# Kernel optimization log

Measured on AMD Instinct MI355X. Metric: run time of the kernel, lower is better.

Reference implementation:

```python
import jax, jax.numpy as jnp
import numpy as np

DIM, DH, H_HEADS, F, HH, WW = 512, 64, 8, 16, 32, 32
FF_IN = int(DIM * 4 * 2 / 3)  # 1365


def _ln(x, w, b):
    m = x.mean(-1, keepdims=True)
    v = ((x - m) ** 2).mean(-1, keepdims=True)
    return (x - m) * jax.lax.rsqrt(v + 1e-5) * w + b


def _attn(x, ln_w, ln_b, wq, wkv, nkv, nbias, wout, oln_w, oln_b, rel_bias):
    # x: (B, N, D); K/V are single-head (shared across heads) per the source to_kv
    B, N, D = x.shape
    H = nbias.shape[0]
    dh = nkv.shape[-1]
    xn = _ln(x, ln_w, ln_b)
    q = (xn @ wq).reshape(B, N, H, dh).transpose(0, 2, 1, 3) * (dh ** -0.5)
    k, v = jnp.split(xn @ wkv, 2, axis=-1)  # (B, N, dh) each
    nk = jnp.broadcast_to(nkv[0], (B, 1, dh))
    nv = jnp.broadcast_to(nkv[1], (B, 1, dh))
    k = jnp.concatenate([nk, k], axis=1)  # (B, N+1, dh)
    v = jnp.concatenate([nv, v], axis=1)
    sim = jnp.einsum('bhid,bjd->bhij', q, k)  # (B, H, N, N+1)
    bias = jnp.concatenate([jnp.broadcast_to(nbias[:, None, None], (H, N, 1)), rel_bias], axis=-1)
    attn = jax.nn.softmax(sim + bias[None], axis=-1)
    out = jnp.einsum('bhij,bjd->bhid', attn, v)
    out = out.transpose(0, 2, 1, 3).reshape(B, N, H * dh)
    return _ln(out @ wout, oln_w, oln_b)


def _cpb_mlp(coords, w0, b0, w1, b1, w2, b2):
    t = jax.nn.silu(coords @ w0 + b0)
    t = jax.nn.silu(t @ w1 + b1)
    return t @ w2 + b2  # (R, heads)


def _spatial_bias(h, w, w0, b0, w1, b1, w2, b2):
    rh = jnp.arange(-h + 1, h)
    rw = jnp.arange(-w + 1, w)
    gh, gw = jnp.meshgrid(rh, rw, indexing='ij')
    coords = jnp.stack([gh, gw], axis=-1).reshape(-1, 2).astype(jnp.float32)
    table = _cpb_mlp(coords, w0, b0, w1, b1, w2, b2)  # ((2h-1)(2w-1), H)
    ph, pw = jnp.meshgrid(jnp.arange(h), jnp.arange(w), indexing='ij')
    p = jnp.stack([ph, pw], axis=-1).reshape(-1, 2)  # (hw, 2)
    rel = p[:, None] - p[None]  # (hw, hw, 2)
    idx = (rel[..., 0] + h - 1) * (2 * w - 1) + (rel[..., 1] + w - 1)
    return table[idx].transpose(2, 0, 1)  # (H, hw, hw)


def _temporal_bias(f, w0, b0, w1, b1, w2, b2):
    coords = jnp.arange(-f + 1, f, dtype=jnp.float32)[:, None]
    table = _cpb_mlp(coords, w0, b0, w1, b1, w2, b2)  # (2f-1, H)
    idx = jnp.arange(f)[:, None] - jnp.arange(f)[None] + f - 1
    return table[idx].transpose(2, 0, 1)  # (H, f, f)


def _ff(x, win, g, wout):
    # 1x1x1 conv == channel matmul; GEGLU; shift_token; ChanLayerNorm; conv out
    y = jnp.einsum('bcfhw,cd->bdfhw', x, win)
    a, gate = jnp.split(y, 2, axis=1)
    y = a * jax.nn.gelu(gate, approximate=False)
    c = y.shape[1]
    c1 = (c + 1) // 2  # torch.chunk: first chunk gets ceil
    y1, y2 = y[:, :c1], y[:, c1:]
    y2 = jnp.pad(y2, ((0, 0), (0, 0), (1, 0), (0, 0), (0, 0)))[:, :, :-1]
    y = jnp.concatenate([y1, y2], axis=1)
    m = y.mean(1, keepdims=True)
    v = ((y - m) ** 2).mean(1, keepdims=True)
    y = (y - m) * jax.lax.rsqrt(jnp.maximum(v, 1e-5)) * g.reshape(1, -1, 1, 1, 1)
    return jnp.einsum('bcfhw,cd->bdfhw', y, wout)


def setup_inputs() -> dict:
    key = jax.random.key(0)
    ks = jax.random.split(key, 32)
    d2 = DIM // 2
    inner = DH * H_HEADS

    def nrm(k, shape, s=0.02):
        return jax.random.normal(k, shape, jnp.float32) * s

    inp = {'x': jax.random.normal(ks[0], (1, DIM, F, HH, WW), jnp.float32)}
    for pre, i in (('sa', 1), ('ta', 11)):
        inp[pre + '_ln_w'] = jnp.ones(DIM, jnp.float32)
        inp[pre + '_ln_b'] = jnp.zeros(DIM, jnp.float32)
        inp[pre + '_wq'] = nrm(ks[i], (DIM, inner))
        inp[pre + '_wkv'] = nrm(ks[i + 1], (DIM, 2 * DH))
        inp[pre + '_null_kv'] = nrm(ks[i + 2], (2, DH), 1.0)
        inp[pre + '_null_bias'] = nrm(ks[i + 3], (H_HEADS,), 1.0)
        inp[pre + '_wout'] = nrm(ks[i + 4], (inner, DIM))
        inp[pre + '_oln_w'] = jnp.ones(DIM, jnp.float32)
        inp[pre + '_oln_b'] = jnp.zeros(DIM, jnp.float32)
    inp['sp_w0'] = nrm(ks[20], (2, d2), 0.1); inp['sp_b0'] = jnp.zeros(d2, jnp.float32)
    inp['sp_w1'] = nrm(ks[21], (d2, d2), 0.05); inp['sp_b1'] = jnp.zeros(d2, jnp.float32)
    inp['sp_w2'] = nrm(ks[22], (d2, H_HEADS), 0.05); inp['sp_b2'] = jnp.zeros(H_HEADS, jnp.float32)
    inp['tp_w0'] = nrm(ks[23], (1, d2), 0.1); inp['tp_b0'] = jnp.zeros(d2, jnp.float32)
    inp['tp_w1'] = nrm(ks[24], (d2, d2), 0.05); inp['tp_b1'] = jnp.zeros(d2, jnp.float32)
    inp['tp_w2'] = nrm(ks[25], (d2, H_HEADS), 0.05); inp['tp_b2'] = jnp.zeros(H_HEADS, jnp.float32)
    inp['ff_win'] = nrm(ks[26], (DIM, 2 * FF_IN))
    inp['ff_g'] = jnp.ones(FF_IN, jnp.float32)
    inp['ff_wout'] = nrm(ks[27], (FF_IN, DIM))
    return inp


def _forward(x, sa_ln_w, sa_ln_b, sa_wq, sa_wkv, sa_null_kv, sa_null_bias, sa_wout, sa_oln_w, sa_oln_b,
             ta_ln_w, ta_ln_b, ta_wq, ta_wkv, ta_null_kv, ta_null_bias, ta_wout, ta_oln_w, ta_oln_b,
             sp_w0, sp_b0, sp_w1, sp_b1, sp_w2, sp_b2,
             tp_w0, tp_b0, tp_w1, tp_b1, tp_w2, tp_b2,
             ff_win, ff_g, ff_wout):
    b, c, f, h, w = x.shape
    # spatial attention over (h*w) tokens, batched over (b*f)
    xs = x.transpose(0, 2, 3, 4, 1).reshape(b * f, h * w, c)
    sb = _spatial_bias(h, w, sp_w0, sp_b0, sp_w1, sp_b1, sp_w2, sp_b2)
    xs = _attn(xs, sa_ln_w, sa_ln_b, sa_wq, sa_wkv, sa_null_kv, sa_null_bias, sa_wout, sa_oln_w, sa_oln_b, sb) + xs
    xv = xs.reshape(b, f, h, w, c).transpose(0, 4, 1, 2, 3)
    # temporal attention over f tokens, batched over (b*h*w)
    xt = xv.transpose(0, 3, 4, 2, 1).reshape(b * h * w, f, c)
    tb = _temporal_bias(f, tp_w0, tp_b0, tp_w1, tp_b1, tp_w2, tp_b2)
    xt = _attn(xt, ta_ln_w, ta_ln_b, ta_wq, ta_wkv, ta_null_kv, ta_null_bias, ta_wout, ta_oln_w, ta_oln_b, tb) + xt
    xv = xt.reshape(b, h, w, f, c).transpose(0, 4, 3, 1, 2)
    # feed-forward with token shift
    return _ff(xv, ff_win, ff_g, ff_wout) + xv


def reference(x, sa_ln_w, sa_ln_b, sa_wq, sa_wkv, sa_null_kv, sa_null_bias, sa_wout, sa_oln_w, sa_oln_b,
              ta_ln_w, ta_ln_b, ta_wq, ta_wkv, ta_null_kv, ta_null_bias, ta_wout, ta_oln_w, ta_oln_b,
              sp_w0, sp_b0, sp_w1, sp_b1, sp_w2, sp_b2,
              tp_w0, tp_b0, tp_w1, tp_b1, tp_w2, tp_b2,
              ff_win, ff_g, ff_wout):
    return _forward(x, sa_ln_w, sa_ln_b, sa_wq, sa_wkv, sa_null_kv, sa_null_bias, sa_wout, sa_oln_w, sa_oln_b,
                    ta_ln_w, ta_ln_b, ta_wq, ta_wkv, ta_null_kv, ta_null_bias, ta_wout, ta_oln_w, ta_oln_b,
                    sp_w0, sp_b0, sp_w1, sp_b1, sp_w2, sp_b2,
                    tp_w0, tp_b0, tp_w1, tp_b1, tp_w2, tp_b2,
                    ff_win, ff_g, ff_wout)
```

## Files before the change

kernel.cpp:

```cpp
#include <hip/hip_runtime.h>
#include <math.h>

#define TOK 16384
#define DIMC 512
#define FFI 1365
#define CH1 683
#define YSLD 1376
#define KVPAD 1056
#define BSTRIDE 1152
#define MASKB (-30000.f)
#define LOG2E 1.4426950408889634f

typedef unsigned int u32;
typedef unsigned short ushort_t;
typedef __attribute__((ext_vector_type(8))) short bf16x8;
typedef __attribute__((ext_vector_type(4))) float f32x4;

__device__ inline ushort_t f2b(float x) {
    u32 u = __float_as_uint(x);
    u32 r = (u + 0x7fffu + ((u >> 16) & 1u)) >> 16;
    return (ushort_t)r;
}
__device__ inline float b2f(ushort_t u) { return __uint_as_float(((u32)u) << 16); }

__device__ inline float exp2_fast(float x) {
    float r;
    asm("v_exp_f32 %0, %1" : "=v"(r) : "v"(x));
    return r;
}

__device__ inline u32 cvt_pk_bf16(float lo, float hi) {
    u32 r;
    asm("v_cvt_pk_bf16_f32 %0, %1, %2" : "=v"(r) : "v"(lo), "v"(hi));
    return r;
}

__device__ inline void gload_lds16(const void* g, void* l) {
    __builtin_amdgcn_global_load_lds(
        (const __attribute__((address_space(1))) u32*)g,
        (__attribute__((address_space(3))) u32*)l, 16, 0, 0);
}

__device__ inline float gelu_exact(float x) {
    return 0.5f * x * (1.f + erff(x * 0.70710678118654752f));
}

__device__ inline void waitcnt_vm4() {
    asm volatile("s_waitcnt vmcnt(4)" ::: "memory");
    __builtin_amdgcn_sched_barrier(0);
}
__device__ inline void waitcnt_vm0() {
    asm volatile("s_waitcnt vmcnt(0)" ::: "memory");
    __builtin_amdgcn_sched_barrier(0);
}

__global__ __launch_bounds__(256) void cpb_kernel(
    const float* __restrict__ w0, const float* __restrict__ b0,
    const float* __restrict__ w1, const float* __restrict__ b1,
    const float* __restrict__ w2, const float* __restrict__ b2,
    float* __restrict__ table, int mode)
{
    __shared__ float t0[256];
    __shared__ float t1[256];
    int r = blockIdx.x;
    int t = threadIdx.x;
    float c0, c1;
    if (mode == 0) { c0 = (float)(r / 63 - 31); c1 = (float)(r % 63 - 31); }
    else           { c0 = (float)(r - 15);      c1 = 0.f; }
    float a = c0 * w0[t] + b0[t];
    if (mode == 0) a += c1 * w0[256 + t];
    t0[t] = a / (1.f + __expf(-a));
    __syncthreads();
    float s = b1[t];
    for (int k = 0; k < 256; ++k) s += t0[k] * w1[k * 256 + t];
    t1[t] = s / (1.f + __expf(-s));
    __syncthreads();
    if (t < 8) {
        float o = b2[t];
        for (int k = 0; k < 256; ++k) o += t1[k] * w2[k * 8 + t];
        table[r * 8 + t] = o;
    }
}

__global__ __launch_bounds__(256) void bias_sp_kernel(
    const float* __restrict__ tab, const float* __restrict__ nullbias,
    ushort_t* __restrict__ out)
{
    int pi = blockIdx.x, h = blockIdx.y;
    int phi = pi >> 5, pwi = pi & 31;
    ushort_t* row = out + ((size_t)h * 1024 + pi) * BSTRIDE;
    for (int c = threadIdx.x; c < BSTRIDE; c += 256) {
        float v;
        if (c == 0) v = nullbias[h];
        else if (c <= 1024) {
            int pj = c - 1;
            int phj = pj >> 5, pwj = pj & 31;
            int idx = (phi - phj + 31) * 63 + (pwi - pwj + 31);
            v = tab[idx * 8 + h];
        } else v = MASKB;
        row[c] = f2b(v * LOG2E);
    }
}

__global__ __launch_bounds__(256) void kvinit_kernel(
    const float* __restrict__ nullkv, ushort_t* __restrict__ KP, ushort_t* __restrict__ VT)
{
    int f = blockIdx.x, t = threadIdx.x;
    for (int e = t; e < 32 * 64; e += 256) {
        int rr = e >> 6, d = e & 63;
        int row = (rr == 0) ? 0 : (1024 + rr);
        KP[((size_t)f * KVPAD + row) * 64 + d] = (rr == 0) ? f2b(nullkv[d]) : (ushort_t)0;
    }
    for (int e = t; e < 64 * 32; e += 256) {
        int d = e >> 5, cc = e & 31;
        int col = (cc == 0) ? 0 : (1024 + cc);
        VT[((size_t)f * 64 + d) * KVPAD + col] = (cc == 0) ? f2b(nullkv[64 + d]) : (ushort_t)0;
    }
}

__global__ __launch_bounds__(256) void wcvt_kernel(
    const float* __restrict__ W, int ldw, int c0,
    ushort_t* __restrict__ Bt, int Kp, int K, int Ncols,
    const float* __restrict__ gv, int Nwrite)
{
    __shared__ float tile[32][33];
    int nb = blockIdx.x * 32, kb = blockIdx.y * 32;
    int tx = threadIdx.x & 31, ty = threadIdx.x >> 5;
    #pragma unroll
    for (int it = 0; it < 4; ++it) {
        int k = kb + ty + it * 8, n = nb + tx;
        float v = (k < K && n < Ncols) ? W[(size_t)k * ldw + c0 + n] : 0.f;
        if (gv && k < K) v *= gv[k];
        tile[ty + it * 8][tx] = v;
    }
    __syncthreads();
    #pragma unroll
    for (int it = 0; it < 4; ++it) {
        int n = nb + ty + it * 8, k = kb + tx;
        if (n < Nwrite && k < Kp) Bt[(size_t)n * Kp + k] = f2b(tile[tx][ty + it * 8]);
    }
}

__global__ __launch_bounds__(256) void transpose_in_kernel(
    const float* __restrict__ x, float* __restrict__ dst)
{
    __shared__ float tile[32][33];
    int t0b = blockIdx.x * 32, c0b = blockIdx.y * 32;
    int tx = threadIdx.x & 31, ty = threadIdx.x >> 5;
    #pragma unroll
    for (int it = 0; it < 4; ++it) {
        int c = ty + it * 8;
        tile[c][tx] = x[(size_t)(c0b + c) * TOK + t0b + tx];
    }
    __syncthreads();
    #pragma unroll
    for (int it = 0; it < 4; ++it) {
        int tr = ty + it * 8;
        dst[(size_t)(t0b + tr) * DIMC + c0b + tx] = tile[tx][tr];
    }
}

__global__ __launch_bounds__(256) void ln_bf16_kernel(
    const float* __restrict__ in, ushort_t* __restrict__ out,
    const float* __restrict__ w, const float* __restrict__ b)
{
    __shared__ float r1[4], r2[4];
    size_t base = (size_t)blockIdx.x * DIMC;
    int t = threadIdx.x;
    float x0 = in[base + t], x1 = in[base + 256 + t];
    float s = x0 + x1, s2 = x0 * x0 + x1 * x1;
    #pragma unroll
    for (int o = 32; o > 0; o >>= 1) { s += __shfl_down(s, o, 64); s2 += __shfl_down(s2, o, 64); }
    if ((t & 63) == 0) { r1[t >> 6] = s; r2[t >> 6] = s2; }
    __syncthreads();
    float mean = (r1[0] + r1[1] + r1[2] + r1[3]) * (1.f / 512.f);
    float ex2  = (r2[0] + r2[1] + r2[2] + r2[3]) * (1.f / 512.f);
    float rstd = rsqrtf(ex2 - mean * mean + 1e-5f);
    out[base + t]       = f2b((x0 - mean) * rstd * w[t] + b[t]);
    out[base + 256 + t] = f2b((x1 - mean) * rstd * w[256 + t] + b[256 + t]);
}

__global__ __launch_bounds__(256) void ln_add_kernel(
    const float* __restrict__ proj, float* __restrict__ io,
    const float* __restrict__ w, const float* __restrict__ b)
{
    __shared__ float r1[4], r2[4];
    size_t base = (size_t)blockIdx.x * DIMC;
    int t = threadIdx.x;
    float x0 = proj[base + t], x1 = proj[base + 256 + t];
    float s = x0 + x1, s2 = x0 * x0 + x1 * x1;
    #pragma unroll
    for (int o = 32; o > 0; o >>= 1) { s += __shfl_down(s, o, 64); s2 += __shfl_down(s2, o, 64); }
    if ((t & 63) == 0) { r1[t >> 6] = s; r2[t >> 6] = s2; }
    __syncthreads();
    float mean = (r1[0] + r1[1] + r1[2] + r1[3]) * (1.f / 512.f);
    float ex2  = (r2[0] + r2[1] + r2[2] + r2[3]) * (1.f / 512.f);
    float rstd = rsqrtf(ex2 - mean * mean + 1e-5f);
    io[base + t]       += (x0 - mean) * rstd * w[t] + b[t];
    io[base + 256 + t] += (x1 - mean) * rstd * w[256 + t] + b[256 + t];
}

__global__ __launch_bounds__(128) void permute0_kernel(
    const float* __restrict__ src, float* __restrict__ dst)
{
    int rd = blockIdx.x;
    int rs = (rd & 15) * 1024 + (rd >> 4);
    ((float4*)(dst + (size_t)rd * DIMC))[threadIdx.x] =
        ((const float4*)(src + (size_t)rs * DIMC))[threadIdx.x];
}

__global__ __launch_bounds__(128) void permute1_dual_kernel(
    const float* __restrict__ src, float* __restrict__ dst, ushort_t* __restrict__ dstb)
{
    int rd = blockIdx.x;
    int rs = (rd & 1023) * 16 + (rd >> 10);
    float4 v = ((const float4*)(src + (size_t)rs * DIMC))[threadIdx.x];
    ((float4*)(dst + (size_t)rd * DIMC))[threadIdx.x] = v;
    u32 lo = (u32)f2b(v.x) | ((u32)f2b(v.y) << 16);
    u32 hi = (u32)f2b(v.z) | ((u32)f2b(v.w) << 16);
    ((uint2*)(dstb + (size_t)rd * DIMC))[threadIdx.x] = make_uint2(lo, hi);
}

template<int EPI>
__global__ __launch_bounds__(256) void gemm_mfma(
    const ushort_t* __restrict__ A, int lda,
    const ushort_t* __restrict__ Bt, int Kp,
    float* __restrict__ C, ushort_t* __restrict__ Cb, int ldc,
    int M, int N, int K, float scale, int nx,
    const float* __restrict__ stats, const float* __restrict__ g,
    const float* __restrict__ resid, float* __restrict__ outT,
    ushort_t* __restrict__ KPo, ushort_t* __restrict__ VTo)
{
    __shared__ __align__(16) ushort_t As[2][4 * 128 * 8];
    __shared__ __align__(16) ushort_t Bs[2][4 * 128 * 8];
    int lin = blockIdx.x;
    int xcd = lin & 7, idx = lin >> 3;
    int m0 = (xcd * 16 + (idx & 15)) * 128;
    int n0 = (idx >> 4) * 128;
    int tid = threadIdx.x, lane = tid & 63, wid = tid >> 6;
    int wy = wid >> 1, wx = wid & 1, quad = lane >> 4, l16 = lane & 15;
    bool bfull = (n0 + 128 <= N);
    f32x4 acc[4][4];
    #pragma unroll
    for (int i = 0; i < 4; ++i)
        #pragma unroll
        for (int j = 0; j < 4; ++j) { acc[i][j][0]=0.f; acc[i][j][1]=0.f; acc[i][j][2]=0.f; acc[i][j][3]=0.f; }

    auto stageA = [&](int buf, int k0) {
        #pragma unroll
        for (int r = 0; r < 2; ++r) {
            int c = wid * 128 + r * 64 + lane;
            const ushort_t* src = A + (size_t)(m0 + (c & 127)) * lda + k0 + (c >> 7) * 8;
            gload_lds16(src, &As[buf][(wid * 128 + r * 64) * 8]);
        }
    };
    auto stageB = [&](int buf, int k0) {
        #pragma unroll
        for (int r = 0; r < 2; ++r) {
            int c = wid * 128 + r * 64 + lane;
            const ushort_t* src = Bt + (size_t)(n0 + (c & 127)) * Kp + k0 + (c >> 7) * 8;
            gload_lds16(src, &Bs[buf][(wid * 128 + r * 64) * 8]);
        }
    };

    if (bfull) {
        int NT = K >> 5;
        stageA(0, 0); stageB(0, 0);
        if (NT > 1) { stageA(1, 32); stageB(1, 32); }
        for (int t = 0; t < NT; ++t) {
            if (t + 1 < NT) waitcnt_vm4(); else waitcnt_vm0();
            __builtin_amdgcn_s_barrier();
            int cur = t & 1;
            bf16x8 af[4], bfr[4];
            #pragma unroll
            for (int i = 0; i < 4; ++i) af[i] = *(bf16x8*)&As[cur][(quad * 128 + wy * 64 + i * 16 + l16) * 8];
            #pragma unroll
            for (int j = 0; j < 4; ++j) bfr[j] = *(bf16x8*)&Bs[cur][(quad * 128 + wx * 64 + j * 16 + l16) * 8];
            #pragma unroll
            for (int i = 0; i < 4; ++i)
                #pragma unroll
                for (int j = 0; j < 4; ++j)
                    acc[i][j] = __builtin_amdgcn_mfma_f32_16x16x32_bf16(af[i], bfr[j], acc[i][j], 0, 0, 0);
            if (t + 2 < NT) {
                __builtin_amdgcn_s_barrier();
                stageA(cur, (t + 2) * 32); stageB(cur, (t + 2) * 32);
            }
        }
    } else {
        for (int k0 = 0; k0 < K; k0 += 32) {
            if (k0) __syncthreads();
            stageA(0, k0);
            #pragma unroll
            for (int r = 0; r < 2; ++r) {
                int c = tid + r * 256;
                int kg = c >> 7, nloc = c & 127;
                bf16x8 v;
                if (n0 + nloc < N) v = *(const bf16x8*)(Bt + (size_t)(n0 + nloc) * Kp + k0 + kg * 8);
                else { for (int e = 0; e < 8; ++e) v[e] = 0; }
                *(bf16x8*)&Bs[0][c * 8] = v;
            }
            __syncthreads();
            bf16x8 af[4], bfr[4];
            #pragma unroll
            for (int i = 0; i < 4; ++i) af[i] = *(bf16x8*)&As[0][(quad * 128 + wy * 64 + i * 16 + l16) * 8];
            #pragma unroll
            for (int j = 0; j < 4; ++j) bfr[j] = *(bf16x8*)&Bs[0][(quad * 128 + wx * 64 + j * 16 + l16) * 8];
            #pragma unroll
            for (int i = 0; i < 4; ++i)
                #pragma unroll
                for (int j = 0; j < 4; ++j)
                    acc[i][j] = __builtin_amdgcn_mfma_f32_16x16x32_bf16(af[i], bfr[j], acc[i][j], 0, 0, 0);
        }
    }
    #pragma unroll
    for (int i = 0; i < 4; ++i) {
        #pragma unroll
        for (int j = 0; j < 4; ++j) {
            #pragma unroll
            for (int r = 0; r < 4; ++r) {
                int m = m0 + wy * 64 + i * 16 + quad * 4 + r;
                int n = n0 + wx * 64 + j * 16 + l16;
                if (n >= N) continue;
                float v = acc[i][j][r] * scale;
                if (EPI == 0) {
                    C[(size_t)m * ldc + n] = v;
                } else if (EPI == 3) {
                    Cb[(size_t)m * ldc + n] = f2b(v);
                } else if (EPI == 4) {
                    int frame = m >> 10, tt = m & 1023;
                    if (n < 64) KPo[((size_t)frame * KVPAD + 1 + tt) * 64 + n] = f2b(v);
                    else        VTo[((size_t)frame * 64 + (n - 64)) * KVPAD + 1 + tt] = f2b(v);
                } else if (EPI == 5) {
                    float s0 = stats[2 * m], s1 = stats[2 * m + 1];
                    outT[(size_t)n * TOK + m] = v * s1 - s0 * g[n] + resid[(size_t)m * DIMC + n];
                }
            }
        }
    }
}

__global__ __launch_bounds__(256) void ff_gemm_fused(
    const ushort_t* __restrict__ A,
    const ushort_t* __restrict__ BI,
    ushort_t* __restrict__ YS)
{
    __shared__ __align__(16) ushort_t As[2][4 * 128 * 8];
    __shared__ __align__(16) ushort_t Bs[2][4 * 2 * 64 * 8];
    int lin = blockIdx.x;
    int xcd = lin & 7, idx = lin >> 3;
    int m0 = (xcd * 16 + (idx & 15)) * 128;
    int n0 = (idx >> 4) * 64;
    int tid = threadIdx.x, lane = tid & 63, wid = tid >> 6;
    int wy = wid >> 1, wx = wid & 1, quad = lane >> 4, l16 = lane & 15;
    f32x4 aA[4][2], aG[4][2];
    #pragma unroll
    for (int i = 0; i < 4; ++i)
        #pragma unroll
        for (int j = 0; j < 2; ++j) {
            aA[i][j][0]=0.f; aA[i][j][1]=0.f; aA[i][j][2]=0.f; aA[i][j][3]=0.f;
            aG[i][j][0]=0.f; aG[i][j][1]=0.f; aG[i][j][2]=0.f; aG[i][j][3]=0.f;
        }

    auto stage = [&](int buf, int k0) {
        #pragma unroll
        for (int r = 0; r < 2; ++r) {
            int c = wid * 128 + r * 64 + lane;
            gload_lds16(A + (size_t)(m0 + (c & 127)) * 512 + k0 + (c >> 7) * 8,
                        &As[buf][(wid * 128 + r * 64) * 8]);
        }
        #pragma unroll
        for (int r = 0; r < 2; ++r) {
            gload_lds16(BI + (size_t)((n0 + lane) * 2 + r) * 512 + k0 + wid * 8,
                        &Bs[buf][(wid * 128 + r * 64) * 8]);
        }
    };

    stage(0, 0);
    stage(1, 32);
    for (int t = 0; t < 16; ++t) {
        if (t + 1 < 16) waitcnt_vm4(); else waitcnt_vm0();
        __builtin_amdgcn_s_barrier();
        int cur = t & 1;
        bf16x8 af[4], ba[2], bg[2];
        #pragma unroll
        for (int i = 0; i < 4; ++i) af[i] = *(bf16x8*)&As[cur][(quad * 128 + wy * 64 + i * 16 + l16) * 8];
        #pragma unroll
        for (int j = 0; j < 2; ++j) {
            int nn = wx * 32 + j * 16 + l16;
            ba[j] = *(bf16x8*)&Bs[cur][(quad * 128 + nn) * 8];
            bg[j] = *(bf16x8*)&Bs[cur][(quad * 128 + 64 + nn) * 8];
        }
        #pragma unroll
        for (int i = 0; i < 4; ++i)
            #pragma unroll
            for (int j = 0; j < 2; ++j) {
                aA[i][j] = __builtin_amdgcn_mfma_f32_16x16x32_bf16(af[i], ba[j], aA[i][j], 0, 0, 0);
                aG[i][j] = __builtin_amdgcn_mfma_f32_16x16x32_bf16(af[i], bg[j], aG[i][j], 0, 0, 0);
            }
        if (t + 2 < 16) {
            __builtin_amdgcn_s_barrier();
            stage(cur, (t + 2) * 32);
        }
    }
    #pragma unroll
    for (int i = 0; i < 4; ++i) {
        #pragma unroll
        for (int j = 0; j < 2; ++j) {
            #pragma unroll
            for (int r = 0; r < 4; ++r) {
                int m = m0 + wy * 64 + i * 16 + quad * 4 + r;
                int n = n0 + wx * 32 + j * 16 + l16;
                if (n >= FFI) {
                    if (n < YSLD) YS[(size_t)m * YSLD + n] = 0;
                    continue;
                }
                float v = aA[i][j][r] * gelu_exact(aG[i][j][r]);
                int dr = (n < CH1) ? m : m + 1024;
                if (dr < TOK) YS[(size_t)dr * YSLD + n] = f2b(v);
                if (n >= CH1 && m < 1024) YS[(size_t)m * YSLD + n] = 0;
            }
        }
    }
}

__global__ __launch_bounds__(256) void attn_sp_mfma(
    const ushort_t* __restrict__ Q,
    const ushort_t* __restrict__ KP,
    const ushort_t* __restrict__ VT,
    const ushort_t* __restrict__ BIASX,
    ushort_t* __restrict__ O)
{
    __shared__ __align__(16) ushort_t Ks[128 * 64];
    __shared__ __align__(16) ushort_t Vs[64 * 128];
    int lin = blockIdx.x;
    int xcd = lin & 7, idx = lin >> 3;
    int qt = xcd * 8 + (idx & 7);
    int frame = idx >> 3;
    int q0 = qt * 16;
    int tid = threadIdx.x, lane = tid & 63, wid = tid >> 6;
    int quad = lane >> 4, l16 = lane & 15;

    bf16x8 aQ[2][2];
    const ushort_t* brow[2];
    #pragma unroll
    for (int i = 0; i < 2; ++i) {
        int h = wid * 2 + i;
        const ushort_t* qp = Q + (size_t)(frame * 1024 + q0 + l16) * 512 + h * 64 + quad * 8;
        aQ[i][0] = *(const bf16x8*)qp;
        aQ[i][1] = *(const bf16x8*)(qp + 32);
        brow[i] = BIASX + ((size_t)h * 1024 + q0 + l16) * BSTRIDE;
    }
    f32x4 Oc[2][4];
    f32x4 Oc4[2];
    #pragma unroll
    for (int i = 0; i < 2; ++i) {
        #pragma unroll
        for (int nt = 0; nt < 4; ++nt) { Oc[i][nt][0]=0.f; Oc[i][nt][1]=0.f; Oc[i][nt][2]=0.f; Oc[i][nt][3]=0.f; }
        Oc4[i][0]=0.f; Oc4[i][1]=0.f; Oc4[i][2]=0.f; Oc4[i][3]=0.f;
    }
    bf16x8 vones;
    #pragma unroll
    for (int e = 0; e < 8; ++e) vones[e] = (short)0x3F80;

    int idxA = (((quad & 1) * 32) + l16) * 4;
    int idxB = idxA + 64;
    bool hiq = (quad >= 2);

    for (int jt = 0; jt < 9; ++jt) {
        __syncthreads();
        #pragma unroll
        for (int r = 0; r < 4; ++r) {
            int L = wid * 256 + r * 64 + lane;
            int c = L >> 3, gp = L & 7, gg = gp ^ (c & 7);
            int jj = jt * 128 + c; if (jj > KVPAD - 1) jj = KVPAD - 1;
            gload_lds16(KP + ((size_t)frame * KVPAD + jj) * 64 + gg * 8, &Ks[(wid * 256 + r * 64) * 8]);
        }
        #pragma unroll
        for (int r = 0; r < 4; ++r) {
            int L = wid * 256 + r * 64 + lane;
            int d = L >> 4, cgp = L & 15;
            int cg = (cgp & 8) | ((cgp & 7) ^ (d & 7));
            int col = jt * 128 + cg * 8; if (col > KVPAD - 8) col = KVPAD - 8;
            gload_lds16(VT + ((size_t)frame * 64 + d) * KVPAD + col, &Vs[(wid * 256 + r * 64) * 8]);
        }
        __syncthreads();

        #pragma unroll
        for (int i = 0; i < 2; ++i) {
            f32x4 S[8];
            #pragma unroll
            for (int j = 0; j < 8; ++j) { S[j][0]=0.f; S[j][1]=0.f; S[j][2]=0.f; S[j][3]=0.f; }
            __builtin_amdgcn_s_setprio(1);
            #pragma unroll
            for (int j = 0; j < 8; ++j) {
                int c = j * 16 + l16;
                #pragma unroll
                for (int ks = 0; ks < 2; ++ks) {
                    bf16x8 kb = *(bf16x8*)&Ks[(c * 8 + ((ks * 4 + quad) ^ (c & 7))) * 8];
                    S[j] = __builtin_amdgcn_mfma_f32_16x16x32_bf16(kb, aQ[i][ks], S[j], 0, 0, 0);
                }
            }
            __builtin_amdgcn_s_setprio(0);
            #pragma unroll
            for (int j = 0; j < 8; ++j) {
                int kbase = jt * 128 + j * 16 + quad * 4;
                uint2 bv = *(const uint2*)(brow[i] + kbase);
                S[j][0] = exp2_fast(S[j][0] + __uint_as_float(bv.x << 16));
                S[j][1] = exp2_fast(S[j][1] + __uint_as_float(bv.x & 0xffff0000u));
                S[j][2] = exp2_fast(S[j][2] + __uint_as_float(bv.y << 16));
                S[j][3] = exp2_fast(S[j][3] + __uint_as_float(bv.y & 0xffff0000u));
            }
            __builtin_amdgcn_s_setprio(1);
            #pragma unroll
            for (int ks = 0; ks < 4; ++ks) {
                int jl = 2 * ks, jh = 2 * ks + 1;
                u32 pxl = cvt_pk_bf16(S[jl][0], S[jl][1]);
                u32 pyl = cvt_pk_bf16(S[jl][2], S[jl][3]);
                u32 pxh = cvt_pk_bf16(S[jh][0], S[jh][1]);
                u32 pyh = cvt_pk_bf16(S[jh][2], S[jh][3]);
                u32 a0 = (u32)__builtin_amdgcn_ds_bpermute(idxA, (int)pxl);
                u32 a1 = (u32)__builtin_amdgcn_ds_bpermute(idxA, (int)pxh);
                u32 b0 = (u32)__builtin_amdgcn_ds_bpermute(idxA, (int)pyl);
                u32 b1 = (u32)__builtin_amdgcn_ds_bpermute(idxA, (int)pyh);
                u32 c0 = (u32)__builtin_amdgcn_ds_bpermute(idxB, (int)pxl);
                u32 c1 = (u32)__builtin_amdgcn_ds_bpermute(idxB, (int)pxh);
                u32 d0 = (u32)__builtin_amdgcn_ds_bpermute(idxB, (int)pyl);
                u32 d1 = (u32)__builtin_amdgcn_ds_bpermute(idxB, (int)pyh);
                union { u32 w[4]; bf16x8 v; } pa;
                pa.w[0] = hiq ? a1 : a0;
                pa.w[1] = hiq ? b1 : b0;
                pa.w[2] = hiq ? c1 : c0;
                pa.w[3] = hiq ? d1 : d0;
                #pragma unroll
                for (int nt = 0; nt < 4; ++nt) {
                    int d = nt * 16 + l16;
                    int cg = ks * 4 + quad;
                    int phys = (cg & 8) | ((cg & 7) ^ (d & 7));
                    bf16x8 vb = *(bf16x8*)&Vs[(d * 16 + phys) * 8];
                    Oc[i][nt] = __builtin_amdgcn_mfma_f32_16x16x32_bf16(pa.v, vb, Oc[i][nt], 0, 0, 0);
                }
                Oc4[i] = __builtin_amdgcn_mfma_f32_16x16x32_bf16(pa.v, vones, Oc4[i], 0, 0, 0);
            }
            __builtin_amdgcn_s_setprio(0);
        }
    }
    #pragma unroll
    for (int i = 0; i < 2; ++i) {
        int h = wid * 2 + i;
        #pragma unroll
        for (int r = 0; r < 4; ++r) {
            float linv = 1.f / Oc4[i][r];
            int ql = quad * 4 + r;
            #pragma unroll
            for (int nt = 0; nt < 4; ++nt) {
                int d = nt * 16 + l16;
                O[(size_t)(frame * 1024 + q0 + ql) * 512 + h * 64 + d] = f2b(Oc[i][nt][r] * linv);
            }
        }
    }
}

__global__ __launch_bounds__(256) void attn_tp_kernel(
    const ushort_t* __restrict__ q, const ushort_t* __restrict__ kv,
    const float* __restrict__ nullkv, const float* __restrict__ nullbias,
    const float* __restrict__ table, ushort_t* __restrict__ out)
{
    __shared__ float qs[16][512];
    __shared__ float ks[17][64];
    __shared__ float vs[17][64];
    __shared__ float sc[8][16][17];
    int b = blockIdx.x;
    int t = threadIdx.x;
    for (int e = t; e < 16 * 512; e += 256) {
        int f = e >> 9, c = e & 511;
        qs[f][c] = b2f(q[(size_t)(b * 16 + f) * 512 + c]);
    }
    for (int e = t; e < 17 * 64; e += 256) {
        int j = e >> 6, d = e & 63;
        ks[j][d] = (j == 0) ? nullkv[d]      : b2f(kv[(size_t)(b * 16 + j - 1) * 128 + d]);
        vs[j][d] = (j == 0) ? nullkv[64 + d] : b2f(kv[(size_t)(b * 16 + j - 1) * 128 + 64 + d]);
    }
    __syncthreads();
    for (int e = t; e < 8 * 16 * 17; e += 256) {
        int h = e / 272, rem = e - h * 272;
        int i = rem / 17, j = rem - i * 17;
        float acc = 0.f;
        for (int d = 0; d < 64; ++d) acc += qs[i][h * 64 + d] * ks[j][d];
        float bias = ((j == 0) ? nullbias[h] : table[(i - (j - 1) + 15) * 8 + h]) * LOG2E;
        sc[h][i][j] = acc + bias;
    }
    __syncthreads();
    if (t < 128) {
        int h = t >> 4, i = t & 15;
        float mx = -1e30f;
        for (int j = 0; j < 17; ++j) mx = fmaxf(mx, sc[h][i][j]);
        float s = 0.f;
        for (int j = 0; j < 17; ++j) { float p = exp2_fast(sc[h][i][j] - mx); sc[h][i][j] = p; s += p; }
        float inv = 1.f / s;
        for (int j = 0; j < 17; ++j) sc[h][i][j] *= inv;
    }
    __syncthreads();
    for (int e = t; e < 16 * 512; e += 256) {
        int i = e >> 9, c = e & 511;
        int h = c >> 6, d = c & 63;
        float acc = 0.f;
        #pragma unroll
        for (int j = 0; j < 17; ++j) acc += sc[h][i][j] * vs[j][d];
        out[(size_t)(b * 16 + i) * 512 + c] = f2b(acc);
    }
}

__global__ __launch_bounds__(256) void rowstats_bf16_kernel(
    const ushort_t* __restrict__ YS, float* __restrict__ stats)
{
    __shared__ float r1[4], r2[4];
    int r = blockIdx.x, t = threadIdx.x;
    const ushort_t* row = YS + (size_t)r * YSLD;
    float s = 0.f, s2 = 0.f;
    for (int c = t; c < FFI; c += 256) {
        float v = b2f(row[c]);
        s += v; s2 += v * v;
    }
    #pragma unroll
    for (int o = 32; o > 0; o >>= 1) { s += __shfl_down(s, o, 64); s2 += __shfl_down(s2, o, 64); }
    if ((t & 63) == 0) { r1[t >> 6] = s; r2[t >> 6] = s2; }
    __syncthreads();
    float S  = r1[0] + r1[1] + r1[2] + r1[3];
    float S2 = r2[0] + r2[1] + r2[2] + r2[3];
    float mean = S * (1.f / 1365.f);
    float var  = S2 * (1.f / 1365.f) - mean * mean;
    float rstd = rsqrtf(fmaxf(var, 1e-5f));
    if (t == 0) { stats[2 * r] = mean * rstd; stats[2 * r + 1] = rstd; }
}

__global__ __launch_bounds__(64) void colsum_kernel(
    const ushort_t* __restrict__ Wt, float* __restrict__ colsum)
{
    int n = blockIdx.x, t = threadIdx.x;
    const ushort_t* row = Wt + (size_t)n * YSLD;
    float s = 0.f;
    for (int k = t; k < YSLD; k += 64) s += b2f(row[k]);
    #pragma unroll
    for (int o = 32; o > 0; o >>= 1) s += __shfl_down(s, o, 64);
    if (t == 0) colsum[n] = s;
}

extern "C" void kernel_launch(void* const* d_in, const int* in_sizes, int n_in,
                              void* d_out, int out_size, void* d_ws, size_t ws_size,
                              hipStream_t stream)
{
    const float* x          = (const float*)d_in[0];
    const float* sa_ln_w    = (const float*)d_in[1];
    const float* sa_ln_b    = (const float*)d_in[2];
    const float* sa_wq      = (const float*)d_in[3];
    const float* sa_wkv     = (const float*)d_in[4];
    const float* sa_null_kv = (const float*)d_in[5];
    const float* sa_null_b  = (const float*)d_in[6];
    const float* sa_wout    = (const float*)d_in[7];
    const float* sa_oln_w   = (const float*)d_in[8];
    const float* sa_oln_b   = (const float*)d_in[9];
    const float* ta_ln_w    = (const float*)d_in[10];
    const float* ta_ln_b    = (const float*)d_in[11];
    const float* ta_wq      = (const float*)d_in[12];
    const float* ta_wkv     = (const float*)d_in[13];
    const float* ta_null_kv = (const float*)d_in[14];
    const float* ta_null_b  = (const float*)d_in[15];
    const float* ta_wout    = (const float*)d_in[16];
    const float* ta_oln_w   = (const float*)d_in[17];
    const float* ta_oln_b   = (const float*)d_in[18];
    const float* sp_w0      = (const float*)d_in[19];
    const float* sp_b0      = (const float*)d_in[20];
    const float* sp_w1      = (const float*)d_in[21];
    const float* sp_b1      = (const float*)d_in[22];
    const float* sp_w2      = (const float*)d_in[23];
    const float* sp_b2      = (const float*)d_in[24];
    const float* tp_w0      = (const float*)d_in[25];
    const float* tp_b0      = (const float*)d_in[26];
    const float* tp_w1      = (const float*)d_in[27];
    const float* tp_b1      = (const float*)d_in[28];
    const float* tp_w2      = (const float*)d_in[29];
    const float* tp_b2      = (const float*)d_in[30];
    const float* ff_win     = (const float*)d_in[31];
    const float* ff_g       = (const float*)d_in[32];
    const float* ff_wout    = (const float*)d_in[33];

    char* ws = (char*)d_ws;
    float*    RES   = (float*)(ws + 0);
    ushort_t* XN16  = (ushort_t*)(ws + 33554432);
    ushort_t* Q16   = (ushort_t*)(ws + 50331648);
    float*    RT    = (float*)(ws + 50331648);
    ushort_t* YS    = (ushort_t*)(ws + 50331648);
    ushort_t* WSA   = (ushort_t*)(ws + 67108864);
    ushort_t* KP    = (ushort_t*)(ws + 83886080);
    ushort_t* VTb   = (ushort_t*)(ws + 86048768);
    ushort_t* KV16  = (ushort_t*)(ws + 83886080);
    ushort_t* WTA   = (ushort_t*)(ws + 90439680);
    ushort_t* AO16  = (ushort_t*)(ws + 92274688);
    ushort_t* BI    = (ushort_t*)(ws + 96468992);
    ushort_t* WFFB  = (ushort_t*)(ws + 99352576);
    ushort_t* BIAS16= (ushort_t*)(ws + 109051904);
    float*    PRJ   = (float*)(ws + 109051904);
    ushort_t* Q16t  = (ushort_t*)(ws + 109051904);
    float*    STATS = (float*)(ws + 142606336);
    float*    SPT   = (float*)(ws + 142737408);
    float*    COLSUM= (float*)(ws + 142737408);
    float*    TPT   = (float*)(ws + 142864448);

    ushort_t* WQ_T  = WSA;
    ushort_t* WKV_T = WSA + 262144;
    ushort_t* WO_T  = WSA + 327680;
    ushort_t* tWQ_T  = WTA;
    ushort_t* tWKV_T = WTA + 262144;
    ushort_t* tWO_T  = WTA + 327680;

    dim3 blk(256);
    const float QSCL = 0.125f * LOG2E;

    cpb_kernel<<<dim3(3969), blk, 0, stream>>>(sp_w0, sp_b0, sp_w1, sp_b1, sp_w2, sp_b2, SPT, 0);
    cpb_kernel<<<dim3(31),   blk, 0, stream>>>(tp_w0, tp_b0, tp_w1, tp_b1, tp_w2, tp_b2, TPT, 1);
    bias_sp_kernel<<<dim3(1024, 8), blk, 0, stream>>>(SPT, sa_null_b, BIAS16);
    kvinit_kernel<<<dim3(16), blk, 0, stream>>>(sa_null_kv, KP, VTb);

    wcvt_kernel<<<dim3(16, 16), blk, 0, stream>>>(sa_wq, 512, 0, WQ_T, 512, 512, 512, nullptr, 512);
    wcvt_kernel<<<dim3(4, 16),  blk, 0, stream>>>(sa_wkv, 128, 0, WKV_T, 512, 512, 128, nullptr, 128);
    wcvt_kernel<<<dim3(16, 16), blk, 0, stream>>>(sa_wout, 512, 0, WO_T, 512, 512, 512, nullptr, 512);
    transpose_in_kernel<<<dim3(512, 16), blk, 0, stream>>>(x, RES);
    ln_bf16_kernel<<<dim3(TOK), blk, 0, stream>>>(RES, XN16, sa_ln_w, sa_ln_b);
    gemm_mfma<3><<<dim3(512), blk, 0, stream>>>(XN16, 512, WQ_T, 512,
        nullptr, Q16, 512, TOK, 512, 512, QSCL, 4, nullptr, nullptr, nullptr, nullptr, nullptr, nullptr);
    gemm_mfma<4><<<dim3(128), blk, 0, stream>>>(XN16, 512, WKV_T, 512,
        nullptr, nullptr, 0, TOK, 128, 512, 1.0f, 1, nullptr, nullptr, nullptr, nullptr, KP, VTb);
    attn_sp_mfma<<<dim3(1024), blk, 0, stream>>>(Q16, KP, VTb, BIAS16, AO16);
    gemm_mfma<0><<<dim3(512), blk, 0, stream>>>(AO16, 512, WO_T, 512,
        PRJ, nullptr, 512, TOK, 512, 512, 1.0f, 4, nullptr, nullptr, nullptr, nullptr, nullptr, nullptr);
    ln_add_kernel<<<dim3(TOK), blk, 0, stream>>>(PRJ, RES, sa_oln_w, sa_oln_b);

    permute0_kernel<<<dim3(TOK), dim3(128), 0, stream>>>(RES, RT);
    wcvt_kernel<<<dim3(16, 16), blk, 0, stream>>>(ta_wq, 512, 0, tWQ_T, 512, 512, 512, nullptr, 512);
    wcvt_kernel<<<dim3(4, 16),  blk, 0, stream>>>(ta_wkv, 128, 0, tWKV_T, 512, 512, 128, nullptr, 128);
    wcvt_kernel<<<dim3(16, 16), blk, 0, stream>>>(ta_wout, 512, 0, tWO_T, 512, 512, 512, nullptr, 512);
    ln_bf16_kernel<<<dim3(TOK), blk, 0, stream>>>(RT, XN16, ta_ln_w, ta_ln_b);
    gemm_mfma<3><<<dim3(512), blk, 0, stream>>>(XN16, 512, tWQ_T, 512,
        nullptr, Q16t, 512, TOK, 512, 512, QSCL, 4, nullptr, nullptr, nullptr, nullptr, nullptr, nullptr);
    gemm_mfma<3><<<dim3(128), blk, 0, stream>>>(XN16, 512, tWKV_T, 512,
        nullptr, KV16, 128, TOK, 128, 512, 1.0f, 1, nullptr, nullptr, nullptr, nullptr, nullptr, nullptr);
    attn_tp_kernel<<<dim3(1024), blk, 0, stream>>>(Q16t, KV16, ta_null_kv, ta_null_b, TPT, AO16);
    gemm_mfma<0><<<dim3(512), blk, 0, stream>>>(AO16, 512, tWO_T, 512,
        PRJ, nullptr, 512, TOK, 512, 512, 1.0f, 4, nullptr, nullptr, nullptr, nullptr, nullptr, nullptr);
    ln_add_kernel<<<dim3(TOK), blk, 0, stream>>>(PRJ, RT, ta_oln_w, ta_oln_b);
    permute1_dual_kernel<<<dim3(TOK), dim3(128), 0, stream>>>(RT, RES, XN16);

    wcvt_kernel<<<dim3(44, 16), blk, 0, stream>>>(ff_win, 2730, 0,   BI,       1024, 512, FFI, nullptr, 1408);
    wcvt_kernel<<<dim3(44, 16), blk, 0, stream>>>(ff_win, 2730, FFI, BI + 512, 1024, 512, FFI, nullptr, 1408);
    wcvt_kernel<<<dim3(16, 43), blk, 0, stream>>>(ff_wout, 512, 0, WFFB, YSLD, FFI, 512, ff_g, 512);
    colsum_kernel<<<dim3(512), dim3(64), 0, stream>>>(WFFB, COLSUM);
    ff_gemm_fused<<<dim3(2816), blk, 0, stream>>>(XN16, BI, YS);
    rowstats_bf16_kernel<<<dim3(TOK), blk, 0, stream>>>(YS, STATS);
    gemm_mfma<5><<<dim3(512), blk, 0, stream>>>(YS, YSLD, WFFB, YSLD,
        nullptr, nullptr, 0, TOK, 512, YSLD, 1.0f, 4, STATS, COLSUM, RES, (float*)d_out, nullptr, nullptr);
}
```

Baseline: 843.1 us.

## Batch CPB MLP rows, triple-buffer GEMM staging, vectorize temporal attention

The CPB MLP kernel now processes 16 coordinate rows per block, so each w1 weight load is reused across rows and far fewer blocks are launched. Both MFMA GEMM kernels move from double to triple-buffered LDS staging with precomputed incrementing global pointers. This drops one barrier per K-step and lets the next tile's loads be issued before the current tile's compute. The temporal attention kernel uses vectorized bf16 loads, float4 dot products and packed stores. The cost is more LDS per block, which may reduce occupancy, and higher register pressure in the CPB kernel.

Result: slower. 876.7 us (+4.0%).

```diff
diff --git a/kernel.cpp b/kernel.cpp
--- a/kernel.cpp
+++ b/kernel.cpp
@@ -58,27 +58,48 @@
     const float* __restrict__ w0, const float* __restrict__ b0,
     const float* __restrict__ w1, const float* __restrict__ b1,
     const float* __restrict__ w2, const float* __restrict__ b2,
-    float* __restrict__ table, int mode)
-{
-    __shared__ float t0[256];
-    __shared__ float t1[256];
-    int r = blockIdx.x;
+    float* __restrict__ table, int mode, int nrows)
+{
+    __shared__ float t0[16][256];
+    __shared__ float t1[16][256];
+    int r0 = blockIdx.x * 16;
     int t = threadIdx.x;
-    float c0, c1;
-    if (mode == 0) { c0 = (float)(r / 63 - 31); c1 = (float)(r % 63 - 31); }
-    else           { c0 = (float)(r - 15);      c1 = 0.f; }
-    float a = c0 * w0[t] + b0[t];
-    if (mode == 0) a += c1 * w0[256 + t];
-    t0[t] = a / (1.f + __expf(-a));
-    __syncthreads();
-    float s = b1[t];
-    for (int k = 0; k < 256; ++k) s += t0[k] * w1[k * 256 + t];
-    t1[t] = s / (1.f + __expf(-s));
-    __syncthreads();
-    if (t < 8) {
-        float o = b2[t];
-        for (int k = 0; k < 256; ++k) o += t1[k] * w2[k * 8 + t];
-        table[r * 8 + t] = o;
+    float w0t = w0[t], b0t = b0[t];
+    float w0t2 = (mode == 0) ? w0[256 + t] : 0.f;
+    #pragma unroll
+    for (int rr = 0; rr < 16; ++rr) {
+        int r = r0 + rr; if (r >= nrows) r = nrows - 1;
+        float c0, c1;
+        if (mode == 0) { c0 = (float)(r / 63 - 31); c1 = (float)(r % 63 - 31); }
+        else           { c0 = (float)(r - 15);      c1 = 0.f; }
+        float a = c0 * w0t + b0t;
+        if (mode == 0) a += c1 * w0t2;
+        t0[rr][t] = a / (1.f + __expf(-a));
+    }
+    __syncthreads();
+    float b1t = b1[t];
+    float acc[16];
+    #pragma unroll
+    for (int rr = 0; rr < 16; ++rr) acc[rr] = b1t;
+    for (int k = 0; k < 256; ++k) {
+        float w = w1[k * 256 + t];
+        #pragma unroll
+        for (int rr = 0; rr < 16; ++rr) acc[rr] += t0[rr][k] * w;
+    }
+    #pragma unroll
+    for (int rr = 0; rr < 16; ++rr) {
+        float s = acc[rr];
+        t1[rr][t] = s / (1.f + __expf(-s));
+    }
+    __syncthreads();
+    if (t < 128) {
+        int rr = t >> 3, oo = t & 7;
+        int r = r0 + rr;
+        if (r < nrows) {
+            float o = b2[oo];
+            for (int k = 0; k < 256; ++k) o += t1[rr][k] * w2[k * 8 + oo];
+            table[r * 8 + oo] = o;
+        }
     }
 }
 
@@ -231,8 +252,8 @@
     const float* __restrict__ resid, float* __restrict__ outT,
     ushort_t* __restrict__ KPo, ushort_t* __restrict__ VTo)
 {
-    __shared__ __align__(16) ushort_t As[2][4 * 128 * 8];
-    __shared__ __align__(16) ushort_t Bs[2][4 * 128 * 8];
+    __shared__ __align__(16) ushort_t As[3][4 * 128 * 8];
+    __shared__ __align__(16) ushort_t Bs[3][4 * 128 * 8];
     int lin = blockIdx.x;
     int xcd = lin & 7, idx = lin >> 3;
     int m0 = (xcd * 16 + (idx & 15)) * 128;
@@ -246,31 +267,28 @@
         #pragma unroll
         for (int j = 0; j < 4; ++j) { acc[i][j][0]=0.f; acc[i][j][1]=0.f; acc[i][j][2]=0.f; acc[i][j][3]=0.f; }
 
-    auto stageA = [&](int buf, int k0) {
-        #pragma unroll
-        for (int r = 0; r < 2; ++r) {
-            int c = wid * 128 + r * 64 + lane;
-            const ushort_t* src = A + (size_t)(m0 + (c & 127)) * lda + k0 + (c >> 7) * 8;
-            gload_lds16(src, &As[buf][(wid * 128 + r * 64) * 8]);
-        }
-    };
-    auto stageB = [&](int buf, int k0) {
-        #pragma unroll
-        for (int r = 0; r < 2; ++r) {
-            int c = wid * 128 + r * 64 + lane;
-            const ushort_t* src = Bt + (size_t)(n0 + (c & 127)) * Kp + k0 + (c >> 7) * 8;
-            gload_lds16(src, &Bs[buf][(wid * 128 + r * 64) * 8]);
-        }
-    };
-
     if (bfull) {
         int NT = K >> 5;
-        stageA(0, 0); stageB(0, 0);
-        if (NT > 1) { stageA(1, 32); stageB(1, 32); }
+        int c0 = wid * 128 + lane, c1 = wid * 128 + 64 + lane;
+        const ushort_t* gA0 = A + (size_t)(m0 + (c0 & 127)) * lda + (c0 >> 7) * 8;
+        const ushort_t* gA1 = A + (size_t)(m0 + (c1 & 127)) * lda + (c1 >> 7) * 8;
+        const ushort_t* gB0 = Bt + (size_t)(n0 + (c0 & 127)) * Kp + (c0 >> 7) * 8;
+        const ushort_t* gB1 = Bt + (size_t)(n0 + (c1 & 127)) * Kp + (c1 >> 7) * 8;
+        const int lo0 = (wid * 128) * 8, lo1 = (wid * 128 + 64) * 8;
+        auto stage = [&](int buf) {
+            gload_lds16(gA0, &As[buf][lo0]);
+            gload_lds16(gA1, &As[buf][lo1]);
+            gload_lds16(gB0, &Bs[buf][lo0]);
+            gload_lds16(gB1, &Bs[buf][lo1]);
+            gA0 += 32; gA1 += 32; gB0 += 32; gB1 += 32;
+        };
+        stage(0);
+        if (NT > 1) stage(1);
+        int cur = 0, nxt = 2;
         for (int t = 0; t < NT; ++t) {
             if (t + 1 < NT) waitcnt_vm4(); else waitcnt_vm0();
             __builtin_amdgcn_s_barrier();
-            int cur = t & 1;
+            if (t + 2 < NT) { stage(nxt); nxt = (nxt == 2) ? 0 : nxt + 1; }
             bf16x8 af[4], bfr[4];
             #pragma unroll
             for (int i = 0; i < 4; ++i) af[i] = *(bf16x8*)&As[cur][(quad * 128 + wy * 64 + i * 16 + l16) * 8];
@@ -281,15 +299,17 @@
                 #pragma unroll
                 for (int j = 0; j < 4; ++j)
                     acc[i][j] = __builtin_amdgcn_mfma_f32_16x16x32_bf16(af[i], bfr[j], acc[i][j], 0, 0, 0);
-            if (t + 2 < NT) {
-                __builtin_amdgcn_s_barrier();
-                stageA(cur, (t + 2) * 32); stageB(cur, (t + 2) * 32);
-            }
+            cur = (cur == 2) ? 0 : cur + 1;
         }
     } else {
         for (int k0 = 0; k0 < K; k0 += 32) {
             if (k0) __syncthreads();
-            stageA(0, k0);
+            #pragma unroll
+            for (int r = 0; r < 2; ++r) {
+                int c = wid * 128 + r * 64 + lane;
+                const ushort_t* src = A + (size_t)(m0 + (c & 127)) * lda + k0 + (c >> 7) * 8;
+                gload_lds16(src, &As[0][(wid * 128 + r * 64) * 8]);
+            }
             #pragma unroll
             for (int r = 0; r < 2; ++r) {
                 int c = tid + r * 256;
@@ -344,8 +364,8 @@
     const ushort_t* __restrict__ BI,
     ushort_t* __restrict__ YS)
 {
-    __shared__ __align__(16) ushort_t As[2][4 * 128 * 8];
-    __shared__ __align__(16) ushort_t Bs[2][4 * 2 * 64 * 8];
+    __shared__ __align__(16) ushort_t As[3][4 * 128 * 8];
+    __shared__ __align__(16) ushort_t Bs[3][4 * 2 * 64 * 8];
     int lin = blockIdx.x;
     int xcd = lin & 7, idx = lin >> 3;
     int m0 = (xcd * 16 + (idx & 15)) * 128;
@@ -361,26 +381,26 @@
             aG[i][j][0]=0.f; aG[i][j][1]=0.f; aG[i][j][2]=0.f; aG[i][j][3]=0.f;
         }
 
-    auto stage = [&](int buf, int k0) {
-        #pragma unroll
-        for (int r = 0; r < 2; ++r) {
-            int c = wid * 128 + r * 64 + lane;
-            gload_lds16(A + (size_t)(m0 + (c & 127)) * 512 + k0 + (c >> 7) * 8,
-                        &As[buf][(wid * 128 + r * 64) * 8]);
-        }
-        #pragma unroll
-        for (int r = 0; r < 2; ++r) {
-            gload_lds16(BI + (size_t)((n0 + lane) * 2 + r) * 512 + k0 + wid * 8,
-                        &Bs[buf][(wid * 128 + r * 64) * 8]);
-        }
+    int c0 = wid * 128 + lane, c1 = wid * 128 + 64 + lane;
+    const ushort_t* gA0 = A + (size_t)(m0 + (c0 & 127)) * 512 + (c0 >> 7) * 8;
+    const ushort_t* gA1 = A + (size_t)(m0 + (c1 & 127)) * 512 + (c1 >> 7) * 8;
+    const ushort_t* gB0 = BI + (size_t)((n0 + lane) * 2 + 0) * 512 + wid * 8;
+    const ushort_t* gB1 = BI + (size_t)((n0 + lane) * 2 + 1) * 512 + wid * 8;
+    const int lo0 = (wid * 128) * 8, lo1 = (wid * 128 + 64) * 8;
+    auto stage = [&](int buf) {
+        gload_lds16(gA0, &As[buf][lo0]);
+        gload_lds16(gA1, &As[buf][lo1]);
+        gload_lds16(gB0, &Bs[buf][lo0]);
+        gload_lds16(gB1, &Bs[buf][lo1]);
+        gA0 += 32; gA1 += 32; gB0 += 32; gB1 += 32;
     };
 
-    stage(0, 0);
-    stage(1, 32);
+    stage(0); stage(1);
+    int cur = 0, nxt = 2;
     for (int t = 0; t < 16; ++t) {
         if (t + 1 < 16) waitcnt_vm4(); else waitcnt_vm0();
         __builtin_amdgcn_s_barrier();
-        int cur = t & 1;
+        if (t + 2 < 16) { stage(nxt); nxt = (nxt == 2) ? 0 : nxt + 1; }
         bf16x8 af[4], ba[2], bg[2];
         #pragma unroll
         for (int i = 0; i < 4; ++i) af[i] = *(bf16x8*)&As[cur][(quad * 128 + wy * 64 + i * 16 + l16) * 8];
@@ -397,10 +417,7 @@
                 aA[i][j] = __builtin_amdgcn_mfma_f32_16x16x32_bf16(af[i], ba[j], aA[i][j], 0, 0, 0);
                 aG[i][j] = __builtin_amdgcn_mfma_f32_16x16x32_bf16(af[i], bg[j], aG[i][j], 0, 0, 0);
             }
-        if (t + 2 < 16) {
-            __builtin_amdgcn_s_barrier();
-            stage(cur, (t + 2) * 32);
-        }
+        cur = (cur == 2) ? 0 : cur + 1;
     }
     #pragma unroll
     for (int i = 0; i < 4; ++i) {
@@ -571,9 +588,14 @@
     __shared__ float sc[8][16][17];
     int b = blockIdx.x;
     int t = threadIdx.x;
-    for (int e = t; e < 16 * 512; e += 256) {
-        int f = e >> 9, c = e & 511;
-        qs[f][c] = b2f(q[(size_t)(b * 16 + f) * 512 + c]);
+    for (int e = t; e < 16 * 64; e += 256) {
+        int f = e >> 6, c8 = e & 63;
+        uint4 v = *(const uint4*)(q + (size_t)(b * 16 + f) * 512 + c8 * 8);
+        float* dst = &qs[f][c8 * 8];
+        dst[0] = b2f((ushort_t)(v.x & 0xffffu)); dst[1] = b2f((ushort_t)(v.x >> 16));
+        dst[2] = b2f((ushort_t)(v.y & 0xffffu)); dst[3] = b2f((ushort_t)(v.y >> 16));
+        dst[4] = b2f((ushort_t)(v.z & 0xffffu)); dst[5] = b2f((ushort_t)(v.z >> 16));
+        dst[6] = b2f((ushort_t)(v.w & 0xffffu)); dst[7] = b2f((ushort_t)(v.w >> 16));
     }
     for (int e = t; e < 17 * 64; e += 256) {
         int j = e >> 6, d = e & 63;
@@ -585,7 +607,16 @@
         int h = e / 272, rem = e - h * 272;
         int i = rem / 17, j = rem - i * 17;
         float acc = 0.f;
-        for (int d = 0; d < 64; ++d) acc += qs[i][h * 64 + d] * ks[j][d];
+        const float4* qp = (const float4*)&qs[i][h * 64];
+        const float4* kp = (const float4*)&ks[j][0];
+        #pragma unroll
+        for (int d4 = 0; d4 < 16; ++d4) {
+            float4 qv = qp[d4], kv4 = kp[d4];
+            acc += qv.x * kv4.x;
+            acc += qv.y * kv4.y;
+            acc += qv.z * kv4.z;
+            acc += qv.w * kv4.w;
+        }
         float bias = ((j == 0) ? nullbias[h] : table[(i - (j - 1) + 15) * 8 + h]) * LOG2E;
         sc[h][i][j] = acc + bias;
     }
@@ -600,13 +631,19 @@
         for (int j = 0; j < 17; ++j) sc[h][i][j] *= inv;
     }
     __syncthreads();
-    for (int e = t; e < 16 * 512; e += 256) {
-        int i = e >> 9, c = e & 511;
-        int h = c >> 6, d = c & 63;
-        float acc = 0.f;
-        #pragma unroll
-        for (int j = 0; j < 17; ++j) acc += sc[h][i][j] * vs[j][d];
-        out[(size_t)(b * 16 + i) * 512 + c] = f2b(acc);
+    for (int e = t; e < 16 * 128; e += 256) {
+        int i = e >> 7, c4 = e & 127;
+        int h = c4 >> 4, d4 = c4 & 15;
+        float ax = 0.f, ay = 0.f, az = 0.f, aw = 0.f;
+        #pragma unroll
+        for (int j = 0; j < 17; ++j) {
+            float p = sc[h][i][j];
+            float4 vv = *(const float4*)&vs[j][d4 * 4];
+            ax += p * vv.x; ay += p * vv.y; az += p * vv.z; aw += p * vv.w;
+        }
+        u32 lo = (u32)f2b(ax) | ((u32)f2b(ay) << 16);
+        u32 hi = (u32)f2b(az) | ((u32)f2b(aw) << 16);
+        *(uint2*)(out + (size_t)(b * 16 + i) * 512 + c4 * 4) = make_uint2(lo, hi);
     }
 }
 
@@ -716,8 +753,8 @@
     dim3 blk(256);
     const float QSCL = 0.125f * LOG2E;
 
-    cpb_kernel<<<dim3(3969), blk, 0, stream>>>(sp_w0, sp_b0, sp_w1, sp_b1, sp_w2, sp_b2, SPT, 0);
-    cpb_kernel<<<dim3(31),   blk, 0, stream>>>(tp_w0, tp_b0, tp_w1, tp_b1, tp_w2, tp_b2, TPT, 1);
+    cpb_kernel<<<dim3(249), blk, 0, stream>>>(sp_w0, sp_b0, sp_w1, sp_b1, sp_w2, sp_b2, SPT, 0, 3969);
+    cpb_kernel<<<dim3(2),   blk, 0, stream>>>(tp_w0, tp_b0, tp_w1, tp_b1, tp_w2, tp_b2, TPT, 1, 31);
     bias_sp_kernel<<<dim3(1024, 8), blk, 0, stream>>>(SPT, sa_null_b, BIAS16);
     kvinit_kernel<<<dim3(16), blk, 0, stream>>>(sa_null_kv, KP, VTb);
 
```
